# Kernel tuning notes

Hardware: AMD Instinct MI355X
Metric: run time of the kernel (lower is better)

The kernel has to match this reference:

```python
import jax, jax.numpy as jnp
import numpy as np

EPS = 1e-9  # Dice BatchNormalization epsilon


def dice(x, alpha):
    # Keras BatchNormalization(axis=-1, center=False, scale=False) in training
    # mode: normalize over all axes except the last using batch statistics.
    mean = jnp.mean(x, axis=(0, 1), keepdims=True)
    var = jnp.var(x, axis=(0, 1), keepdims=True)
    x_normed = (x - mean) * jax.lax.rsqrt(var + EPS)
    p = jax.nn.sigmoid(x_normed)
    return alpha * (1.0 - p) * x + p * x


def setup_inputs() -> dict:
    key = jax.random.key(0)
    ks = jax.random.split(key, 11)
    B, T, D = 512, 2048, 20
    keys_ = jax.random.normal(ks[0], (B, T, D), dtype=jnp.float32)
    query = jax.random.normal(ks[1], (B, 1, D), dtype=jnp.float32)
    mask = jax.random.randint(ks[2], (B, T), 0, 2) > 0
    # DNN tower weights: hidden dims 80 -> 32 -> 16, attention head 16 -> 1
    W0 = jax.random.normal(ks[3], (80, 32), dtype=jnp.float32) * 0.1
    b0 = jax.random.normal(ks[4], (32,), dtype=jnp.float32) * 0.1
    a0 = jax.random.normal(ks[5], (32,), dtype=jnp.float32) * 0.1
    W1 = jax.random.normal(ks[6], (32, 16), dtype=jnp.float32) * 0.1
    b1 = jax.random.normal(ks[7], (16,), dtype=jnp.float32) * 0.1
    a1 = jax.random.normal(ks[8], (16,), dtype=jnp.float32) * 0.1
    wk = jax.random.normal(ks[9], (16, 1), dtype=jnp.float32) * 0.1
    bk = jax.random.normal(ks[10], (1,), dtype=jnp.float32) * 0.1
    return {"keys": keys_, "query": query, "mask": mask,
            "W0": W0, "b0": b0, "a0": a0,
            "W1": W1, "b1": b1, "a1": a1,
            "wk": wk, "bk": bk}


def reference(keys, query, mask, W0, b0, a0, W1, b1, a1, wk, bk):
    B, T, D = keys.shape
    # repeat query along the key/time axis: [B,1,D] -> [B,T,D]
    queries = jnp.broadcast_to(query, (B, T, D))
    # local-activation features: [B,T,4D] = [B,T,80]
    att = jnp.concatenate([queries, keys, queries - keys, queries * keys], axis=-1)
    # DNN tower with Dice activations (dropout is identity at inference)
    h = dice(att @ W0 + b0, a0)   # [B,T,32]
    h = dice(h @ W1 + b1, a1)     # [B,T,16]
    score = h @ wk + bk           # [B,T,1]
    outputs = jnp.transpose(score, (0, 2, 1))  # [B,1,T]
    # NOTE: the original code computes the masked scores into self.outputs but
    # then (weight_normalization=False, return_score=False) overwrites it with
    # matmul(outputs, keys) using the UNMASKED scores -- we reproduce that.
    return jnp.matmul(outputs, keys)  # [B,1,D]
```

## Files before the change

### kernel.cpp

```cpp
#include <hip/hip_runtime.h>


#define BB 512
#define TT 2048
#define DD 20
#define C0 32
#define C1 16

#define NTH 256
#define TILE 256
#define CHUNK 1024
#define SPB (CHUNK / TILE)
#define NBLK (TT / CHUNK)
#define GRID (BB * NBLK)
#define NSLOT 8

#define WS_P1 0
#define WS_P2 512
#define WS_ZERO_N 768
#define WS_BLOB 896
#define BLOB_J 24
#define BLOB_B (C0 * BLOB_J)

#define PIN(x) asm volatile("" : "+v"(x))
#define AGLOAD(p) \
    __hip_atomic_load((p), __ATOMIC_RELAXED, __HIP_MEMORY_SCOPE_AGENT)

#define GAS __attribute__((address_space(1)))
#define LAS __attribute__((address_space(3)))

__device__ __forceinline__ float fast_sigmoid(float x) {
    return __builtin_amdgcn_rcpf(1.0f + __expf(-x));
}

__device__ __forceinline__ void stage_tile(const float* __restrict__ gsrc,
                                           float* lbuf, int wave, int lane) {
    const float* gw = gsrc + wave * 1280 + lane * 4;
    float* lw_ = lbuf + wave * 1280;
#pragma unroll
    for (int u = 0; u < 5; ++u)
        __builtin_amdgcn_global_load_lds((const GAS void*)(gw + u * 256),
                                         (LAS void*)(lw_ + u * 256), 16, 0,
                                         0);
}

__device__ __forceinline__ void load_row_lds(const float* __restrict__ row,
                                             float* kk) {
    const float4* r4 = (const float4*)row;
    float4 a = r4[0], b = r4[1], c = r4[2], d = r4[3], e = r4[4];
    kk[0] = a.x; kk[1] = a.y; kk[2] = a.z; kk[3] = a.w;
    kk[4] = b.x; kk[5] = b.y; kk[6] = b.z; kk[7] = b.w;
    kk[8] = c.x; kk[9] = c.y; kk[10] = c.z; kk[11] = c.w;
    kk[12] = d.x; kk[13] = d.y; kk[14] = d.z; kk[15] = d.w;
    kk[16] = e.x; kk[17] = e.y; kk[18] = e.z; kk[19] = e.w;
}

__global__ void prep_kernel(const float* __restrict__ query,
                            const float* __restrict__ W0,
                            const float* __restrict__ b0,
                            float* __restrict__ blob, float* __restrict__ ws,
                            float* __restrict__ out) {
    const int b = blockIdx.x * 2 + (threadIdx.x >> 5);
    const int j = threadIdx.x & 31;
    if (blockIdx.x == 0) {
        for (int i = threadIdx.x; i < WS_ZERO_N; i += 64) ws[i] = 0.f;
    }
    if (j < DD) out[b * DD + j] = 0.f;
    float cj = b0[j];
    float* dst = blob + (size_t)b * BLOB_B + j * BLOB_J;
#pragma unroll
    for (int d = 0; d < DD; ++d) {
        float w_q = W0[d * C0 + j];
        float w_k = W0[(DD + d) * C0 + j];
        float w_d = W0[(2 * DD + d) * C0 + j];
        float w_p = W0[(3 * DD + d) * C0 + j];
        float qd = query[b * DD + d];
        dst[d] = w_k - w_d + qd * w_p;
        cj = fmaf(qd, w_q + w_d, cj);
    }
    dst[20] = cj;
}

__device__ __forceinline__ void finalize0(int tid, float* __restrict__ ws,
                                          float2* __restrict__ lss0) {
    if (tid < C0) {
        float sv = 0.f, qv = 0.f;
#pragma unroll
        for (int k = 0; k < NSLOT; ++k) {
            sv += AGLOAD(&ws[WS_P1 + k * (2 * C0) + tid]);
            qv += AGLOAD(&ws[WS_P1 + k * (2 * C0) + C0 + tid]);
        }
        const float invN = 1.0f / (float)(BB * TT);
        float mean = sv * invN;
        float var = qv * invN - mean * mean;
        float sc = rsqrtf(var + 1e-9f);
        lss0[tid] = make_float2(sc, -mean * sc);
    }
}

__device__ __forceinline__ void finalize1(int tid, float* __restrict__ ws,
                                          const float* __restrict__ a1,
                                          const float* __restrict__ wk,
                                          float4* __restrict__ ld1v) {
    if (tid < C1) {
        float sv = 0.f, qv = 0.f;
#pragma unroll
        for (int k = 0; k < NSLOT; ++k) {
            sv += AGLOAD(&ws[WS_P2 + k * (2 * C1) + tid]);
            qv += AGLOAD(&ws[WS_P2 + k * (2 * C1) + C1 + tid]);
        }
        const float invN = 1.0f / (float)(BB * TT);
        float mean = sv * invN;
        float var = qv * invN - mean * mean;
        float sc = rsqrtf(var + 1e-9f);
        ld1v[tid] = make_float4(sc, -mean * sc, a1[tid], wk[tid]);
    }
}

__global__ __launch_bounds__(NTH, 2) void pass1_kernel(
    const float* __restrict__ keys, const float* __restrict__ blob,
    float* __restrict__ ws) {
    const int batch = blockIdx.x >> 1, chunk = blockIdx.x & 1;
    const int slot = blockIdx.x & (NSLOT - 1);
    const int tid = threadIdx.x, wave = tid >> 6, lane = tid & 63;
    const float* bA = blob + (size_t)batch * BLOB_B;
    const float* kbase = keys + ((size_t)batch * TT + chunk * CHUNK) * DD;

    __shared__ __align__(16) float kbuf[2][TILE * DD];

    float s[C0], q[C0];
#pragma unroll
    for (int j = 0; j < C0; ++j) { s[j] = 0.f; q[j] = 0.f; }

    stage_tile(kbase, kbuf[0], wave, lane);
    __syncthreads();
#pragma unroll 1
    for (int st = 0; st < SPB; ++st) {
        const int buf = st & 1;
        if (st + 1 < SPB)
            stage_tile(kbase + (size_t)(st + 1) * TILE * DD, kbuf[buf ^ 1],
                       wave, lane);
        float kk[DD];
        load_row_lds(&kbuf[buf][tid * DD], kk);
#pragma unroll
        for (int d = 0; d < DD; ++d) PIN(kk[d]);
#pragma unroll
        for (int j = 0; j < C0; ++j) {
            const float* wr = bA + j * BLOB_J;
            float hh = wr[20];
#pragma unroll
            for (int d = 0; d < DD; ++d) hh = fmaf(kk[d], wr[d], hh);
            s[j] += hh;
            q[j] = fmaf(hh, hh, q[j]);
        }
        __syncthreads();
    }
    float redv = 0.f;
#pragma unroll
    for (int v = 0; v < 2 * C0; ++v) {
        float val = (v < C0) ? s[v] : q[v - C0];
#pragma unroll
        for (int o = 32; o >= 1; o >>= 1) val += __shfl_xor(val, o);
        if (lane == v) redv = val;
    }
    atomicAdd(&ws[WS_P1 + slot * (2 * C0) + lane], redv);
}

__global__ __launch_bounds__(NTH, 2) void pass2_kernel(
    const float* __restrict__ keys, const float* __restrict__ blob,
    const float* __restrict__ a0, const float* __restrict__ W1,
    const float* __restrict__ b1, float* __restrict__ ws) {
    const int batch = blockIdx.x >> 1, chunk = blockIdx.x & 1;
    const int slot = blockIdx.x & (NSLOT - 1);
    const int tid = threadIdx.x, wave = tid >> 6, lane = tid & 63;
    const float* bA = blob + (size_t)batch * BLOB_B;
    const float* kbase = keys + ((size_t)batch * TT + chunk * CHUNK) * DD;

    __shared__ __align__(16) float kbuf[2][TILE * DD];
    __shared__ float2 lss0[C0];

    finalize0(tid, ws, lss0);

    float s1[C1], q1[C1];
#pragma unroll
    for (int c = 0; c < C1; ++c) { s1[c] = 0.f; q1[c] = 0.f; }

    stage_tile(kbase, kbuf[0], wave, lane);
    __syncthreads();
#pragma unroll 1
    for (int st = 0; st < SPB; ++st) {
        const int buf = st & 1;
        if (st + 1 < SPB)
            stage_tile(kbase + (size_t)(st + 1) * TILE * DD, kbuf[buf ^ 1],
                       wave, lane);
        float kk[DD];
        load_row_lds(&kbuf[buf][tid * DD], kk);
#pragma unroll
        for (int d = 0; d < DD; ++d) PIN(kk[d]);
        float h1[C1];
#pragma unroll
        for (int c = 0; c < C1; ++c) h1[c] = 0.f;
#pragma unroll
        for (int j = 0; j < C0; ++j) {
            const float* wr = bA + j * BLOB_J;
            const float* ur = W1 + j * C1;
            const float2 ss = lss0[j];
            const float al = a0[j];
            float hh = wr[20];
#pragma unroll
            for (int d = 0; d < DD; ++d) hh = fmaf(kk[d], wr[d], hh);
            float pr = fast_sigmoid(fmaf(hh, ss.x, ss.y));
            float h0d = hh * fmaf(pr, 1.0f - al, al);
#pragma unroll
            for (int c = 0; c < C1; ++c) h1[c] = fmaf(h0d, ur[c], h1[c]);
        }
#pragma unroll
        for (int c = 0; c < C1; ++c) {
            float v = h1[c] + b1[c];
            s1[c] += v;
            q1[c] = fmaf(v, v, q1[c]);
        }
        __syncthreads();
    }
    float redv = 0.f;
#pragma unroll
    for (int v = 0; v < 2 * C1; ++v) {
        float val = (v < C1) ? s1[v] : q1[v - C1];
#pragma unroll
        for (int o = 32; o >= 1; o >>= 1) val += __shfl_xor(val, o);
        if (lane == v) redv = val;
    }
    if (lane < 2 * C1)
        atomicAdd(&ws[WS_P2 + slot * (2 * C1) + lane], redv);
}

__global__ __launch_bounds__(NTH, 2) void pass3_kernel(
    const float* __restrict__ keys, const float* __restrict__ blob,
    const float* __restrict__ a0, const float* __restrict__ W1,
    const float* __restrict__ b1, const float* __restrict__ a1,
    const float* __restrict__ wk, const float* __restrict__ bk,
    float* __restrict__ ws, float* __restrict__ out) {
    const int batch = blockIdx.x >> 1, chunk = blockIdx.x & 1;
    const int tid = threadIdx.x, wave = tid >> 6, lane = tid & 63;
    const float* bA = blob + (size_t)batch * BLOB_B;
    const float* kbase = keys + ((size_t)batch * TT + chunk * CHUNK) * DD;

    __shared__ __align__(16) float kbuf[2][TILE * DD];
    __shared__ float2 lss0[C0];
    __shared__ float4 ld1v[C1];
    __shared__ float red[4][DD];

    finalize0(tid, ws, lss0);
    finalize1(tid, ws, a1, wk, ld1v);

    const float bkv = bk[0];
    float oacc[DD];
#pragma unroll
    for (int d = 0; d < DD; ++d) oacc[d] = 0.f;

    stage_tile(kbase, kbuf[0], wave, lane);
    __syncthreads();
#pragma unroll 1
    for (int st = 0; st < SPB; ++st) {
        const int buf = st & 1;
        if (st + 1 < SPB)
            stage_tile(kbase + (size_t)(st + 1) * TILE * DD, kbuf[buf ^ 1],
                       wave, lane);
        float kk[DD];
        load_row_lds(&kbuf[buf][tid * DD], kk);
#pragma unroll
        for (int d = 0; d < DD; ++d) PIN(kk[d]);
        float h1[C1];
#pragma unroll
        for (int c = 0; c < C1; ++c) h1[c] = 0.f;
#pragma unroll
        for (int j = 0; j < C0; ++j) {
            const float* wr = bA + j * BLOB_J;
            const float* ur = W1 + j * C1;
            const float2 ss = lss0[j];
            const float al = a0[j];
            float hh = wr[20];
#pragma unroll
            for (int d = 0; d < DD; ++d) hh = fmaf(kk[d], wr[d], hh);
            float pr = fast_sigmoid(fmaf(hh, ss.x, ss.y));
            float h0d = hh * fmaf(pr, 1.0f - al, al);
#pragma unroll
            for (int c = 0; c < C1; ++c) h1[c] = fmaf(h0d, ur[c], h1[c]);
        }
        float score = bkv;
#pragma unroll
        for (int c = 0; c < C1; ++c) {
            float v = h1[c] + b1[c];
            float4 dv = ld1v[c];
            float pr = fast_sigmoid(fmaf(v, dv.x, dv.y));
            float hd = v * fmaf(pr, 1.0f - dv.z, dv.z);
            score = fmaf(hd, dv.w, score);
        }
#pragma unroll
        for (int d = 0; d < DD; ++d) oacc[d] = fmaf(score, kk[d], oacc[d]);
        __syncthreads();
    }
    float redv = 0.f;
#pragma unroll
    for (int v = 0; v < DD; ++v) {
        float val = oacc[v];
#pragma unroll
        for (int o = 32; o >= 1; o >>= 1) val += __shfl_xor(val, o);
        if (lane == v) redv = val;
    }
    if (lane < DD) red[wave][lane] = redv;
    __syncthreads();
    if (tid < DD)
        atomicAdd(&out[batch * DD + tid],
                  red[0][tid] + red[1][tid] + red[2][tid] + red[3][tid]);
}

extern "C" void kernel_launch(void* const* d_in, const int* in_sizes, int n_in,
                              void* d_out, int out_size, void* d_ws,
                              size_t ws_size, hipStream_t stream) {
    const float* keys = (const float*)d_in[0];
    const float* query = (const float*)d_in[1];
    const float* W0 = (const float*)d_in[3];
    const float* b0 = (const float*)d_in[4];
    const float* a0 = (const float*)d_in[5];
    const float* W1 = (const float*)d_in[6];
    const float* b1 = (const float*)d_in[7];
    const float* a1 = (const float*)d_in[8];
    const float* wk = (const float*)d_in[9];
    const float* bk = (const float*)d_in[10];
    float* out = (float*)d_out;
    float* ws = (float*)d_ws;
    float* blob = ws + WS_BLOB;

    prep_kernel<<<BB / 2, 64, 0, stream>>>(query, W0, b0, blob, ws, out);
    pass1_kernel<<<GRID, NTH, 0, stream>>>(keys, blob, ws);
    pass2_kernel<<<GRID, NTH, 0, stream>>>(keys, blob, a0, W1, b1, ws);
    pass3_kernel<<<GRID, NTH, 0, stream>>>(keys, blob, a0, W1, b1, a1, wk,
                                           bk, ws, out);
}
```

Before: 319.6 us.

## Cache layer activations in bf16 across passes instead of recomputing from keys

Pass1 now writes the first-layer pre-activations to workspace as bf16, and pass2 reads them back instead of recomputing the 20x32 projection from keys. Pass2 in turn writes the second-layer pre-activations in bf16 for pass3 to read. The cached path is taken only when the workspace is large enough, with the old recompute path kept as a fallback. The LDS staging with global_load_lds is replaced by direct per-thread row loads, and the chunk size is halved, which doubles the grid. In exchange, compute is traded for extra global traffic of about 64MB written and read, and bf16 rounding adds error to the activations.

```diff
diff --git a/kernel.cpp b/kernel.cpp
--- a/kernel.cpp
+++ b/kernel.cpp
@@ -1,4 +1,5 @@
 #include <hip/hip_runtime.h>
+#include <hip/hip_bf16.h>
 
 
 #define BB 512
@@ -8,11 +9,9 @@
 #define C1 16
 
 #define NTH 256
-#define TILE 256
-#define CHUNK 1024
-#define SPB (CHUNK / TILE)
-#define NBLK (TT / CHUNK)
-#define GRID (BB * NBLK)
+#define CHUNK 512
+#define NPART (TT / CHUNK)
+#define GRID (BB * NPART)
 #define NSLOT 8
 
 #define WS_P1 0
@@ -21,38 +20,42 @@
 #define WS_BLOB 896
 #define BLOB_J 24
 #define BLOB_B (C0 * BLOB_J)
+#define H0_OFFB ((size_t)(WS_BLOB + BB * BLOB_B) * 4)
+#define H0_BYTES ((size_t)BB * TT * C0 * 2)
+#define H1_OFFB (H0_OFFB + H0_BYTES)
+#define H1_BYTES ((size_t)BB * TT * C1 * 2)
+#define WS_NEED (H1_OFFB + H1_BYTES)
 
 #define PIN(x) asm volatile("" : "+v"(x))
 #define AGLOAD(p) \
     __hip_atomic_load((p), __ATOMIC_RELAXED, __HIP_MEMORY_SCOPE_AGENT)
 
-#define GAS __attribute__((address_space(1)))
-#define LAS __attribute__((address_space(3)))
-
 __device__ __forceinline__ float fast_sigmoid(float x) {
     return __builtin_amdgcn_rcpf(1.0f + __expf(-x));
 }
 
-__device__ __forceinline__ void stage_tile(const float* __restrict__ gsrc,
-                                           float* lbuf, int wave, int lane) {
-    const float* gw = gsrc + wave * 1280 + lane * 4;
-    float* lw_ = lbuf + wave * 1280;
-#pragma unroll
-    for (int u = 0; u < 5; ++u)
-        __builtin_amdgcn_global_load_lds((const GAS void*)(gw + u * 256),
-                                         (LAS void*)(lw_ + u * 256), 16, 0,
-                                         0);
-}
-
-__device__ __forceinline__ void load_row_lds(const float* __restrict__ row,
-                                             float* kk) {
-    const float4* r4 = (const float4*)row;
-    float4 a = r4[0], b = r4[1], c = r4[2], d = r4[3], e = r4[4];
+__device__ __forceinline__ void load_krow(const float* __restrict__ row,
+                                          float* kk) {
+    const float4* kr = (const float4*)row;
+    float4 a = kr[0], b = kr[1], c = kr[2], d = kr[3], e = kr[4];
     kk[0] = a.x; kk[1] = a.y; kk[2] = a.z; kk[3] = a.w;
     kk[4] = b.x; kk[5] = b.y; kk[6] = b.z; kk[7] = b.w;
     kk[8] = c.x; kk[9] = c.y; kk[10] = c.z; kk[11] = c.w;
     kk[12] = d.x; kk[13] = d.y; kk[14] = d.z; kk[15] = d.w;
     kk[16] = e.x; kk[17] = e.y; kk[18] = e.z; kk[19] = e.w;
+}
+
+__device__ __forceinline__ unsigned int pkbf(float a, float b) {
+    union { __hip_bfloat16 h[2]; unsigned int u; } cv;
+    cv.h[0] = __float2bfloat16(a);
+    cv.h[1] = __float2bfloat16(b);
+    return cv.u;
+}
+__device__ __forceinline__ float bflo(unsigned int u) {
+    return __uint_as_float(u << 16);
+}
+__device__ __forceinline__ float bfhi(unsigned int u) {
+    return __uint_as_float(u & 0xffff0000u);
 }
 
 __global__ void prep_kernel(const float* __restrict__ query,
@@ -117,43 +120,51 @@
     }
 }
 
+template <bool WRITE>
 __global__ __launch_bounds__(NTH, 2) void pass1_kernel(
     const float* __restrict__ keys, const float* __restrict__ blob,
-    float* __restrict__ ws) {
-    const int batch = blockIdx.x >> 1, chunk = blockIdx.x & 1;
+    float* __restrict__ ws, unsigned int* __restrict__ h0c) {
+    const int batch = blockIdx.x >> 2, part = blockIdx.x & 3;
     const int slot = blockIdx.x & (NSLOT - 1);
-    const int tid = threadIdx.x, wave = tid >> 6, lane = tid & 63;
+    const int tid = threadIdx.x, lane = tid & 63;
     const float* bA = blob + (size_t)batch * BLOB_B;
-    const float* kbase = keys + ((size_t)batch * TT + chunk * CHUNK) * DD;
-
-    __shared__ __align__(16) float kbuf[2][TILE * DD];
+    const float* kbase = keys + ((size_t)batch * TT + part * CHUNK) * DD;
 
     float s[C0], q[C0];
 #pragma unroll
     for (int j = 0; j < C0; ++j) { s[j] = 0.f; q[j] = 0.f; }
 
-    stage_tile(kbase, kbuf[0], wave, lane);
-    __syncthreads();
 #pragma unroll 1
-    for (int st = 0; st < SPB; ++st) {
-        const int buf = st & 1;
-        if (st + 1 < SPB)
-            stage_tile(kbase + (size_t)(st + 1) * TILE * DD, kbuf[buf ^ 1],
-                       wave, lane);
+    for (int r = 0; r < CHUNK / NTH; ++r) {
+        const int row = r * NTH + tid;
         float kk[DD];
-        load_row_lds(&kbuf[buf][tid * DD], kk);
+        load_krow(kbase + (size_t)row * DD, kk);
 #pragma unroll
         for (int d = 0; d < DD; ++d) PIN(kk[d]);
-#pragma unroll
-        for (int j = 0; j < C0; ++j) {
-            const float* wr = bA + j * BLOB_J;
-            float hh = wr[20];
-#pragma unroll
-            for (int d = 0; d < DD; ++d) hh = fmaf(kk[d], wr[d], hh);
-            s[j] += hh;
-            q[j] = fmaf(hh, hh, q[j]);
-        }
-        __syncthreads();
+        const size_t pos = (size_t)batch * TT + part * CHUNK + row;
+#pragma unroll
+        for (int jg = 0; jg < 4; ++jg) {
+            float h[8];
+#pragma unroll
+            for (int je = 0; je < 8; ++je) {
+                const int j = jg * 8 + je;
+                const float* wr = bA + j * BLOB_J;
+                float hh = wr[20];
+#pragma unroll
+                for (int d = 0; d < DD; ++d) hh = fmaf(kk[d], wr[d], hh);
+                h[je] = hh;
+                s[j] += hh;
+                q[j] = fmaf(hh, hh, q[j]);
+            }
+            if (WRITE) {
+                uint4 u;
+                u.x = pkbf(h[0], h[1]);
+                u.y = pkbf(h[2], h[3]);
+                u.z = pkbf(h[4], h[5]);
+                u.w = pkbf(h[6], h[7]);
+                *reinterpret_cast<uint4*>(h0c + pos * 16 + jg * 4) = u;
+            }
+        }
     }
     float redv = 0.f;
 #pragma unroll
@@ -166,61 +177,98 @@
     atomicAdd(&ws[WS_P1 + slot * (2 * C0) + lane], redv);
 }
 
+template <bool CACHED>
 __global__ __launch_bounds__(NTH, 2) void pass2_kernel(
     const float* __restrict__ keys, const float* __restrict__ blob,
     const float* __restrict__ a0, const float* __restrict__ W1,
-    const float* __restrict__ b1, float* __restrict__ ws) {
-    const int batch = blockIdx.x >> 1, chunk = blockIdx.x & 1;
+    const float* __restrict__ b1, float* __restrict__ ws,
+    const unsigned int* __restrict__ h0c, unsigned int* __restrict__ h1c) {
+    const int batch = blockIdx.x >> 2, part = blockIdx.x & 3;
     const int slot = blockIdx.x & (NSLOT - 1);
-    const int tid = threadIdx.x, wave = tid >> 6, lane = tid & 63;
+    const int tid = threadIdx.x, lane = tid & 63;
     const float* bA = blob + (size_t)batch * BLOB_B;
-    const float* kbase = keys + ((size_t)batch * TT + chunk * CHUNK) * DD;
-
-    __shared__ __align__(16) float kbuf[2][TILE * DD];
+    const float* kbase = keys + ((size_t)batch * TT + part * CHUNK) * DD;
     __shared__ float2 lss0[C0];
-
     finalize0(tid, ws, lss0);
+    __syncthreads();
 
     float s1[C1], q1[C1];
 #pragma unroll
     for (int c = 0; c < C1; ++c) { s1[c] = 0.f; q1[c] = 0.f; }
 
-    stage_tile(kbase, kbuf[0], wave, lane);
-    __syncthreads();
 #pragma unroll 1
-    for (int st = 0; st < SPB; ++st) {
-        const int buf = st & 1;
-        if (st + 1 < SPB)
-            stage_tile(kbase + (size_t)(st + 1) * TILE * DD, kbuf[buf ^ 1],
-                       wave, lane);
-        float kk[DD];
-        load_row_lds(&kbuf[buf][tid * DD], kk);
-#pragma unroll
-        for (int d = 0; d < DD; ++d) PIN(kk[d]);
+    for (int r = 0; r < CHUNK / NTH; ++r) {
+        const int row = r * NTH + tid;
+        const size_t pos = (size_t)batch * TT + part * CHUNK + row;
         float h1[C1];
 #pragma unroll
         for (int c = 0; c < C1; ++c) h1[c] = 0.f;
-#pragma unroll
-        for (int j = 0; j < C0; ++j) {
-            const float* wr = bA + j * BLOB_J;
-            const float* ur = W1 + j * C1;
-            const float2 ss = lss0[j];
-            const float al = a0[j];
-            float hh = wr[20];
-#pragma unroll
-            for (int d = 0; d < DD; ++d) hh = fmaf(kk[d], wr[d], hh);
-            float pr = fast_sigmoid(fmaf(hh, ss.x, ss.y));
-            float h0d = hh * fmaf(pr, 1.0f - al, al);
-#pragma unroll
-            for (int c = 0; c < C1; ++c) h1[c] = fmaf(h0d, ur[c], h1[c]);
-        }
+
+        if (CACHED) {
+            const uint4* hp =
+                reinterpret_cast<const uint4*>(h0c + pos * 16);
+            uint4 u0 = hp[0], u1 = hp[1], u2 = hp[2], u3 = hp[3];
+            unsigned int uw[16] = {u0.x, u0.y, u0.z, u0.w, u1.x, u1.y,
+                                   u1.z, u1.w, u2.x, u2.y, u2.z, u2.w,
+                                   u3.x, u3.y, u3.z, u3.w};
+#pragma unroll
+            for (int jp = 0; jp < 16; ++jp) {
+                const unsigned int u = uw[jp];
+#pragma unroll
+                for (int e = 0; e < 2; ++e) {
+                    const int j = jp * 2 + e;
+                    float hh = e ? bfhi(u) : bflo(u);
+                    const float2 ss = lss0[j];
+                    const float al = a0[j];
+                    float pr = fast_sigmoid(fmaf(hh, ss.x, ss.y));
+                    float gg = hh * fmaf(pr, 1.0f - al, al);
+                    const float* ur = W1 + j * C1;
+#pragma unroll
+                    for (int c = 0; c < C1; ++c)
+                        h1[c] = fmaf(gg, ur[c], h1[c]);
+                }
+            }
+        } else {
+            float kk[DD];
+            load_krow(kbase + (size_t)row * DD, kk);
+#pragma unroll
+            for (int d = 0; d < DD; ++d) PIN(kk[d]);
+#pragma unroll
+            for (int j = 0; j < C0; ++j) {
+                const float* wr = bA + j * BLOB_J;
+                float hh = wr[20];
+#pragma unroll
+                for (int d = 0; d < DD; ++d) hh = fmaf(kk[d], wr[d], hh);
+                const float2 ss = lss0[j];
+                const float al = a0[j];
+                float pr = fast_sigmoid(fmaf(hh, ss.x, ss.y));
+                float gg = hh * fmaf(pr, 1.0f - al, al);
+                const float* ur = W1 + j * C1;
+#pragma unroll
+                for (int c = 0; c < C1; ++c) h1[c] = fmaf(gg, ur[c], h1[c]);
+            }
+        }
+        float vv[C1];
 #pragma unroll
         for (int c = 0; c < C1; ++c) {
-            float v = h1[c] + b1[c];
-            s1[c] += v;
-            q1[c] = fmaf(v, v, q1[c]);
-        }
-        __syncthreads();
+            vv[c] = h1[c] + b1[c];
+            s1[c] += vv[c];
+            q1[c] = fmaf(vv[c], vv[c], q1[c]);
+        }
+        if (CACHED) {
+            uint4 w0, w1;
+            w0.x = pkbf(vv[0], vv[1]);
+            w0.y = pkbf(vv[2], vv[3]);
+            w0.z = pkbf(vv[4], vv[5]);
+            w0.w = pkbf(vv[6], vv[7]);
+            w1.x = pkbf(vv[8], vv[9]);
+            w1.y = pkbf(vv[10], vv[11]);
+            w1.z = pkbf(vv[12], vv[13]);
+            w1.w = pkbf(vv[14], vv[15]);
+            uint4* wp = reinterpret_cast<uint4*>(h1c + pos * 8);
+            wp[0] = w0;
+            wp[1] = w1;
+        }
     }
     float redv = 0.f;
 #pragma unroll
@@ -234,71 +282,81 @@
         atomicAdd(&ws[WS_P2 + slot * (2 * C1) + lane], redv);
 }
 
+template <bool CACHED>
 __global__ __launch_bounds__(NTH, 2) void pass3_kernel(
     const float* __restrict__ keys, const float* __restrict__ blob,
     const float* __restrict__ a0, const float* __restrict__ W1,
     const float* __restrict__ b1, const float* __restrict__ a1,
     const float* __restrict__ wk, const float* __restrict__ bk,
-    float* __restrict__ ws, float* __restrict__ out) {
-    const int batch = blockIdx.x >> 1, chunk = blockIdx.x & 1;
+    float* __restrict__ ws, float* __restrict__ out,
+    const unsigned int* __restrict__ h1c) {
+    const int batch = blockIdx.x >> 2, part = blockIdx.x & 3;
     const int tid = threadIdx.x, wave = tid >> 6, lane = tid & 63;
     const float* bA = blob + (size_t)batch * BLOB_B;
-    const float* kbase = keys + ((size_t)batch * TT + chunk * CHUNK) * DD;
-
-    __shared__ __align__(16) float kbuf[2][TILE * DD];
+    const float* kbase = keys + ((size_t)batch * TT + part * CHUNK) * DD;
     __shared__ float2 lss0[C0];
     __shared__ float4 ld1v[C1];
     __shared__ float red[4][DD];
-
-    finalize0(tid, ws, lss0);
+    if (!CACHED) finalize0(tid, ws, lss0);
     finalize1(tid, ws, a1, wk, ld1v);
+    __syncthreads();
 
     const float bkv = bk[0];
     float oacc[DD];
 #pragma unroll
     for (int d = 0; d < DD; ++d) oacc[d] = 0.f;
 
-    stage_tile(kbase, kbuf[0], wave, lane);
-    __syncthreads();
 #pragma unroll 1
-    for (int st = 0; st < SPB; ++st) {
-        const int buf = st & 1;
-        if (st + 1 < SPB)
-            stage_tile(kbase + (size_t)(st + 1) * TILE * DD, kbuf[buf ^ 1],
-                       wave, lane);
+    for (int r = 0; r < CHUNK / NTH; ++r) {
+        const int row = r * NTH + tid;
+        const size_t pos = (size_t)batch * TT + part * CHUNK + row;
         float kk[DD];
-        load_row_lds(&kbuf[buf][tid * DD], kk);
+        load_krow(kbase + (size_t)row * DD, kk);
 #pragma unroll
         for (int d = 0; d < DD; ++d) PIN(kk[d]);
-        float h1[C1];
-#pragma unroll
-        for (int c = 0; c < C1; ++c) h1[c] = 0.f;
-#pragma unroll
-        for (int j = 0; j < C0; ++j) {
-            const float* wr = bA + j * BLOB_J;
-            const float* ur = W1 + j * C1;
-            const float2 ss = lss0[j];
-            const float al = a0[j];
-            float hh = wr[20];
-#pragma unroll
-            for (int d = 0; d < DD; ++d) hh = fmaf(kk[d], wr[d], hh);
-            float pr = fast_sigmoid(fmaf(hh, ss.x, ss.y));
-            float h0d = hh * fmaf(pr, 1.0f - al, al);
-#pragma unroll
-            for (int c = 0; c < C1; ++c) h1[c] = fmaf(h0d, ur[c], h1[c]);
+        float vv[C1];
+        if (CACHED) {
+            const uint4* hp = reinterpret_cast<const uint4*>(h1c + pos * 8);
+            uint4 u0 = hp[0], u1 = hp[1];
+            vv[0] = bflo(u0.x); vv[1] = bfhi(u0.x);
+            vv[2] = bflo(u0.y); vv[3] = bfhi(u0.y);
+            vv[4] = bflo(u0.z); vv[5] = bfhi(u0.z);
+            vv[6] = bflo(u0.w); vv[7] = bfhi(u0.w);
+            vv[8] = bflo(u1.x); vv[9] = bfhi(u1.x);
+            vv[10] = bflo(u1.y); vv[11] = bfhi(u1.y);
+            vv[12] = bflo(u1.z); vv[13] = bfhi(u1.z);
+            vv[14] = bflo(u1.w); vv[15] = bfhi(u1.w);
+        } else {
+            float h1[C1];
+#pragma unroll
+            for (int c = 0; c < C1; ++c) h1[c] = 0.f;
+#pragma unroll
+            for (int j = 0; j < C0; ++j) {
+                const float* wr = bA + j * BLOB_J;
+                float hh = wr[20];
+#pragma unroll
+                for (int d = 0; d < DD; ++d) hh = fmaf(kk[d], wr[d], hh);
+                const float2 ss = lss0[j];
+                const float al = a0[j];
+                float pr = fast_sigmoid(fmaf(hh, ss.x, ss.y));
+                float gg = hh * fmaf(pr, 1.0f - al, al);
+                const float* ur = W1 + j * C1;
+#pragma unroll
+                for (int c = 0; c < C1; ++c) h1[c] = fmaf(gg, ur[c], h1[c]);
+            }
+#pragma unroll
+            for (int c = 0; c < C1; ++c) vv[c] = h1[c] + b1[c];
         }
         float score = bkv;
 #pragma unroll
         for (int c = 0; c < C1; ++c) {
-            float v = h1[c] + b1[c];
             float4 dv = ld1v[c];
-            float pr = fast_sigmoid(fmaf(v, dv.x, dv.y));
-            float hd = v * fmaf(pr, 1.0f - dv.z, dv.z);
+            float pr = fast_sigmoid(fmaf(vv[c], dv.x, dv.y));
+            float hd = vv[c] * fmaf(pr, 1.0f - dv.z, dv.z);
             score = fmaf(hd, dv.w, score);
         }
 #pragma unroll
         for (int d = 0; d < DD; ++d) oacc[d] = fmaf(score, kk[d], oacc[d]);
-        __syncthreads();
     }
     float redv = 0.f;
 #pragma unroll
@@ -331,10 +389,24 @@
     float* out = (float*)d_out;
     float* ws = (float*)d_ws;
     float* blob = ws + WS_BLOB;
+    unsigned int* h0c = (unsigned int*)((char*)d_ws + H0_OFFB);
+    unsigned int* h1c = (unsigned int*)((char*)d_ws + H1_OFFB);
+    const bool cached = ws_size >= WS_NEED;
 
     prep_kernel<<<BB / 2, 64, 0, stream>>>(query, W0, b0, blob, ws, out);
-    pass1_kernel<<<GRID, NTH, 0, stream>>>(keys, blob, ws);
-    pass2_kernel<<<GRID, NTH, 0, stream>>>(keys, blob, a0, W1, b1, ws);
-    pass3_kernel<<<GRID, NTH, 0, stream>>>(keys, blob, a0, W1, b1, a1, wk,
-                                           bk, ws, out);
-}
+    if (cached) {
+        pass1_kernel<true><<<GRID, NTH, 0, stream>>>(keys, blob, ws, h0c);
+        pass2_kernel<true><<<GRID, NTH, 0, stream>>>(keys, blob, a0, W1, b1,
+                                                     ws, h0c, h1c);
+        pass3_kernel<true><<<GRID, NTH, 0, stream>>>(keys, blob, a0, W1, b1,
+                                                     a1, wk, bk, ws, out,
+                                                     h1c);
+    } else {
+        pass1_kernel<false><<<GRID, NTH, 0, stream>>>(keys, blob, ws, h0c);
+        pass2_kernel<false><<<GRID, NTH, 0, stream>>>(keys, blob, a0, W1, b1,
+                                                      ws, h0c, h1c);
+        pass3_kernel<false><<<GRID, NTH, 0, stream>>>(keys, blob, a0, W1, b1,
+                                                      a1, wk, bk, ws, out,
+                                                      h1c);
+    }
+}
```

New measurement: 364.5 us. 1.14x slower.

## Replace LDS-staged key tiles with direct register double-buffered global loads

Applied to the files above, without the earlier changes.

Removes the global_load_lds staging of key tiles into shared memory, along with the per-tile __syncthreads, in all three passes. Each thread now loads its own 20-float rows straight from global memory as five float4 loads, with two register buffers software-pipelined across its four rows. This drops the LDS traffic and block barriers but gives up coalescing, since each thread reads a separate 80-byte row, and it raises register pressure.

```diff
diff --git a/kernel.cpp b/kernel.cpp
--- a/kernel.cpp
+++ b/kernel.cpp
@@ -8,9 +8,7 @@
 #define C1 16
 
 #define NTH 256
-#define TILE 256
 #define CHUNK 1024
-#define SPB (CHUNK / TILE)
 #define NBLK (TT / CHUNK)
 #define GRID (BB * NBLK)
 #define NSLOT 8
@@ -26,33 +24,31 @@
 #define AGLOAD(p) \
     __hip_atomic_load((p), __ATOMIC_RELAXED, __HIP_MEMORY_SCOPE_AGENT)
 
-#define GAS __attribute__((address_space(1)))
-#define LAS __attribute__((address_space(3)))
-
 __device__ __forceinline__ float fast_sigmoid(float x) {
     return __builtin_amdgcn_rcpf(1.0f + __expf(-x));
 }
 
-__device__ __forceinline__ void stage_tile(const float* __restrict__ gsrc,
-                                           float* lbuf, int wave, int lane) {
-    const float* gw = gsrc + wave * 1280 + lane * 4;
-    float* lw_ = lbuf + wave * 1280;
-#pragma unroll
-    for (int u = 0; u < 5; ++u)
-        __builtin_amdgcn_global_load_lds((const GAS void*)(gw + u * 256),
-                                         (LAS void*)(lw_ + u * 256), 16, 0,
-                                         0);
-}
-
-__device__ __forceinline__ void load_row_lds(const float* __restrict__ row,
-                                             float* kk) {
-    const float4* r4 = (const float4*)row;
-    float4 a = r4[0], b = r4[1], c = r4[2], d = r4[3], e = r4[4];
-    kk[0] = a.x; kk[1] = a.y; kk[2] = a.z; kk[3] = a.w;
-    kk[4] = b.x; kk[5] = b.y; kk[6] = b.z; kk[7] = b.w;
-    kk[8] = c.x; kk[9] = c.y; kk[10] = c.z; kk[11] = c.w;
-    kk[12] = d.x; kk[13] = d.y; kk[14] = d.z; kk[15] = d.w;
-    kk[16] = e.x; kk[17] = e.y; kk[18] = e.z; kk[19] = e.w;
+__device__ __forceinline__ void load5(const float* __restrict__ row,
+                                      float4 (&P)[5]) {
+    const float4* k4 = (const float4*)row;
+    P[0] = k4[0];
+    P[1] = k4[1];
+    P[2] = k4[2];
+    P[3] = k4[3];
+    P[4] = k4[4];
+}
+
+__device__ __forceinline__ void unpack20(const float4 (&P)[5],
+                                         float (&kk)[DD]) {
+#pragma unroll
+    for (int u = 0; u < 5; ++u) {
+        kk[u * 4 + 0] = P[u].x;
+        kk[u * 4 + 1] = P[u].y;
+        kk[u * 4 + 2] = P[u].z;
+        kk[u * 4 + 3] = P[u].w;
+    }
+#pragma unroll
+    for (int d = 0; d < DD; ++d) PIN(kk[d]);
 }
 
 __global__ void prep_kernel(const float* __restrict__ query,
@@ -117,44 +113,45 @@
     }
 }
 
+__device__ __forceinline__ void p1row(const float4 (&P)[5],
+                                      const float* __restrict__ bA,
+                                      float (&s)[C0], float (&q)[C0]) {
+    float kk[DD];
+    unpack20(P, kk);
+#pragma unroll
+    for (int j = 0; j < C0; ++j) {
+        const float* wr = bA + j * BLOB_J;
+        float hh = wr[20];
+#pragma unroll
+        for (int d = 0; d < DD; ++d) hh = fmaf(kk[d], wr[d], hh);
+        s[j] += hh;
+        q[j] = fmaf(hh, hh, q[j]);
+    }
+}
+
 __global__ __launch_bounds__(NTH, 2) void pass1_kernel(
     const float* __restrict__ keys, const float* __restrict__ blob,
     float* __restrict__ ws) {
     const int batch = blockIdx.x >> 1, chunk = blockIdx.x & 1;
     const int slot = blockIdx.x & (NSLOT - 1);
-    const int tid = threadIdx.x, wave = tid >> 6, lane = tid & 63;
+    const int tid = threadIdx.x, lane = tid & 63;
     const float* bA = blob + (size_t)batch * BLOB_B;
     const float* kbase = keys + ((size_t)batch * TT + chunk * CHUNK) * DD;
 
-    __shared__ __align__(16) float kbuf[2][TILE * DD];
-
     float s[C0], q[C0];
 #pragma unroll
     for (int j = 0; j < C0; ++j) { s[j] = 0.f; q[j] = 0.f; }
 
-    stage_tile(kbase, kbuf[0], wave, lane);
-    __syncthreads();
-#pragma unroll 1
-    for (int st = 0; st < SPB; ++st) {
-        const int buf = st & 1;
-        if (st + 1 < SPB)
-            stage_tile(kbase + (size_t)(st + 1) * TILE * DD, kbuf[buf ^ 1],
-                       wave, lane);
-        float kk[DD];
-        load_row_lds(&kbuf[buf][tid * DD], kk);
-#pragma unroll
-        for (int d = 0; d < DD; ++d) PIN(kk[d]);
-#pragma unroll
-        for (int j = 0; j < C0; ++j) {
-            const float* wr = bA + j * BLOB_J;
-            float hh = wr[20];
-#pragma unroll
-            for (int d = 0; d < DD; ++d) hh = fmaf(kk[d], wr[d], hh);
-            s[j] += hh;
-            q[j] = fmaf(hh, hh, q[j]);
-        }
-        __syncthreads();
-    }
+    float4 A[5], B[5];
+    load5(kbase + (size_t)tid * DD, A);
+    load5(kbase + (size_t)(tid + NTH) * DD, B);
+    p1row(A, bA, s, q);
+    load5(kbase + (size_t)(tid + 2 * NTH) * DD, A);
+    p1row(B, bA, s, q);
+    load5(kbase + (size_t)(tid + 3 * NTH) * DD, B);
+    p1row(A, bA, s, q);
+    p1row(B, bA, s, q);
+
     float redv = 0.f;
 #pragma unroll
     for (int v = 0; v < 2 * C0; ++v) {
@@ -164,6 +161,40 @@
         if (lane == v) redv = val;
     }
     atomicAdd(&ws[WS_P1 + slot * (2 * C0) + lane], redv);
+}
+
+__device__ __forceinline__ void p2row(const float4 (&P)[5],
+                                      const float* __restrict__ bA,
+                                      const float* __restrict__ a0,
+                                      const float* __restrict__ W1,
+                                      const float* __restrict__ b1,
+                                      const float2* __restrict__ lss0,
+                                      float (&s1)[C1], float (&q1)[C1]) {
+    float kk[DD];
+    unpack20(P, kk);
+    float h1[C1];
+#pragma unroll
+    for (int c = 0; c < C1; ++c) h1[c] = 0.f;
+#pragma unroll
+    for (int j = 0; j < C0; ++j) {
+        const float* wr = bA + j * BLOB_J;
+        float hh = wr[20];
+#pragma unroll
+        for (int d = 0; d < DD; ++d) hh = fmaf(kk[d], wr[d], hh);
+        const float2 ss = lss0[j];
+        const float al = a0[j];
+        float pr = fast_sigmoid(fmaf(hh, ss.x, ss.y));
+        float gg = hh * fmaf(pr, 1.0f - al, al);
+        const float* ur = W1 + j * C1;
+#pragma unroll
+        for (int c = 0; c < C1; ++c) h1[c] = fmaf(gg, ur[c], h1[c]);
+    }
+#pragma unroll
+    for (int c = 0; c < C1; ++c) {
+        float v = h1[c] + b1[c];
+        s1[c] += v;
+        q1[c] = fmaf(v, v, q1[c]);
+    }
 }
 
 __global__ __launch_bounds__(NTH, 2) void pass2_kernel(
@@ -172,56 +203,27 @@
     const float* __restrict__ b1, float* __restrict__ ws) {
     const int batch = blockIdx.x >> 1, chunk = blockIdx.x & 1;
     const int slot = blockIdx.x & (NSLOT - 1);
-    const int tid = threadIdx.x, wave = tid >> 6, lane = tid & 63;
+    const int tid = threadIdx.x, lane = tid & 63;
     const float* bA = blob + (size_t)batch * BLOB_B;
     const float* kbase = keys + ((size_t)batch * TT + chunk * CHUNK) * DD;
-
-    __shared__ __align__(16) float kbuf[2][TILE * DD];
     __shared__ float2 lss0[C0];
-
     finalize0(tid, ws, lss0);
+    __syncthreads();
 
     float s1[C1], q1[C1];
 #pragma unroll
     for (int c = 0; c < C1; ++c) { s1[c] = 0.f; q1[c] = 0.f; }
 
-    stage_tile(kbase, kbuf[0], wave, lane);
-    __syncthreads();
-#pragma unroll 1
-    for (int st = 0; st < SPB; ++st) {
-        const int buf = st & 1;
-        if (st + 1 < SPB)
-            stage_tile(kbase + (size_t)(st + 1) * TILE * DD, kbuf[buf ^ 1],
-                       wave, lane);
-        float kk[DD];
-        load_row_lds(&kbuf[buf][tid * DD], kk);
-#pragma unroll
-        for (int d = 0; d < DD; ++d) PIN(kk[d]);
-        float h1[C1];
-#pragma unroll
-        for (int c = 0; c < C1; ++c) h1[c] = 0.f;
-#pragma unroll
-        for (int j = 0; j < C0; ++j) {
-            const float* wr = bA + j * BLOB_J;
-            const float* ur = W1 + j * C1;
-            const float2 ss = lss0[j];
-            const float al = a0[j];
-            float hh = wr[20];
-#pragma unroll
-            for (int d = 0; d < DD; ++d) hh = fmaf(kk[d], wr[d], hh);
-            float pr = fast_sigmoid(fmaf(hh, ss.x, ss.y));
-            float h0d = hh * fmaf(pr, 1.0f - al, al);
-#pragma unroll
-            for (int c = 0; c < C1; ++c) h1[c] = fmaf(h0d, ur[c], h1[c]);
-        }
-#pragma unroll
-        for (int c = 0; c < C1; ++c) {
-            float v = h1[c] + b1[c];
-            s1[c] += v;
-            q1[c] = fmaf(v, v, q1[c]);
-        }
-        __syncthreads();
-    }
+    float4 A[5], B[5];
+    load5(kbase + (size_t)tid * DD, A);
+    load5(kbase + (size_t)(tid + NTH) * DD, B);
+    p2row(A, bA, a0, W1, b1, lss0, s1, q1);
+    load5(kbase + (size_t)(tid + 2 * NTH) * DD, A);
+    p2row(B, bA, a0, W1, b1, lss0, s1, q1);
+    load5(kbase + (size_t)(tid + 3 * NTH) * DD, B);
+    p2row(A, bA, a0, W1, b1, lss0, s1, q1);
+    p2row(B, bA, a0, W1, b1, lss0, s1, q1);
+
     float redv = 0.f;
 #pragma unroll
     for (int v = 0; v < 2 * C1; ++v) {
@@ -232,6 +234,43 @@
     }
     if (lane < 2 * C1)
         atomicAdd(&ws[WS_P2 + slot * (2 * C1) + lane], redv);
+}
+
+__device__ __forceinline__ void p3row(
+    const float4 (&P)[5], const float* __restrict__ bA,
+    const float* __restrict__ a0, const float* __restrict__ W1,
+    const float* __restrict__ b1, const float2* __restrict__ lss0,
+    const float4* __restrict__ ld1v, float bkv, float (&oacc)[DD]) {
+    float kk[DD];
+    unpack20(P, kk);
+    float h1[C1];
+#pragma unroll
+    for (int c = 0; c < C1; ++c) h1[c] = 0.f;
+#pragma unroll
+    for (int j = 0; j < C0; ++j) {
+        const float* wr = bA + j * BLOB_J;
+        float hh = wr[20];
+#pragma unroll
+        for (int d = 0; d < DD; ++d) hh = fmaf(kk[d], wr[d], hh);
+        const float2 ss = lss0[j];
+        const float al = a0[j];
+        float pr = fast_sigmoid(fmaf(hh, ss.x, ss.y));
+        float gg = hh * fmaf(pr, 1.0f - al, al);
+        const float* ur = W1 + j * C1;
+#pragma unroll
+        for (int c = 0; c < C1; ++c) h1[c] = fmaf(gg, ur[c], h1[c]);
+    }
+    float score = bkv;
+#pragma unroll
+    for (int c = 0; c < C1; ++c) {
+        float v = h1[c] + b1[c];
+        float4 dv = ld1v[c];
+        float pr = fast_sigmoid(fmaf(v, dv.x, dv.y));
+        float hd = v * fmaf(pr, 1.0f - dv.z, dv.z);
+        score = fmaf(hd, dv.w, score);
+    }
+#pragma unroll
+    for (int d = 0; d < DD; ++d) oacc[d] = fmaf(score, kk[d], oacc[d]);
 }
 
 __global__ __launch_bounds__(NTH, 2) void pass3_kernel(
@@ -244,62 +283,28 @@
     const int tid = threadIdx.x, wave = tid >> 6, lane = tid & 63;
     const float* bA = blob + (size_t)batch * BLOB_B;
     const float* kbase = keys + ((size_t)batch * TT + chunk * CHUNK) * DD;
-
-    __shared__ __align__(16) float kbuf[2][TILE * DD];
     __shared__ float2 lss0[C0];
     __shared__ float4 ld1v[C1];
     __shared__ float red[4][DD];
-
     finalize0(tid, ws, lss0);
     finalize1(tid, ws, a1, wk, ld1v);
+    __syncthreads();
 
     const float bkv = bk[0];
     float oacc[DD];
 #pragma unroll
     for (int d = 0; d < DD; ++d) oacc[d] = 0.f;
 
-    stage_tile(kbase, kbuf[0], wave, lane);
-    __syncthreads();
-#pragma unroll 1
-    for (int st = 0; st < SPB; ++st) {
-        const int buf = st & 1;
-        if (st + 1 < SPB)
-            stage_tile(kbase + (size_t)(st + 1) * TILE * DD, kbuf[buf ^ 1],
-                       wave, lane);
-        float kk[DD];
-        load_row_lds(&kbuf[buf][tid * DD], kk);
-#pragma unroll
-        for (int d = 0; d < DD; ++d) PIN(kk[d]);
-        float h1[C1];
-#pragma unroll
-        for (int c = 0; c < C1; ++c) h1[c] = 0.f;
-#pragma unroll
-        for (int j = 0; j < C0; ++j) {
-            const float* wr = bA + j * BLOB_J;
-            const float* ur = W1 + j * C1;
-            const float2 ss = lss0[j];
-            const float al = a0[j];
-            float hh = wr[20];
-#pragma unroll
-            for (int d = 0; d < DD; ++d) hh = fmaf(kk[d], wr[d], hh);
-            float pr = fast_sigmoid(fmaf(hh, ss.x, ss.y));
-            float h0d = hh * fmaf(pr, 1.0f - al, al);
-#pragma unroll
-            for (int c = 0; c < C1; ++c) h1[c] = fmaf(h0d, ur[c], h1[c]);
-        }
-        float score = bkv;
-#pragma unroll
-        for (int c = 0; c < C1; ++c) {
-            float v = h1[c] + b1[c];
-            float4 dv = ld1v[c];
-            float pr = fast_sigmoid(fmaf(v, dv.x, dv.y));
-            float hd = v * fmaf(pr, 1.0f - dv.z, dv.z);
-            score = fmaf(hd, dv.w, score);
-        }
-#pragma unroll
-        for (int d = 0; d < DD; ++d) oacc[d] = fmaf(score, kk[d], oacc[d]);
-        __syncthreads();
-    }
+    float4 A[5], B[5];
+    load5(kbase + (size_t)tid * DD, A);
+    load5(kbase + (size_t)(tid + NTH) * DD, B);
+    p3row(A, bA, a0, W1, b1, lss0, ld1v, bkv, oacc);
+    load5(kbase + (size_t)(tid + 2 * NTH) * DD, A);
+    p3row(B, bA, a0, W1, b1, lss0, ld1v, bkv, oacc);
+    load5(kbase + (size_t)(tid + 3 * NTH) * DD, B);
+    p3row(A, bA, a0, W1, b1, lss0, ld1v, bkv, oacc);
+    p3row(B, bA, a0, W1, b1, lss0, ld1v, bkv, oacc);
+
     float redv = 0.f;
 #pragma unroll
     for (int v = 0; v < DD; ++v) {
```

Measured after the change: 293.2 us. -8.2%, faster.
